# Performance work log

Measured on AMD Instinct MI355X. Metric: run time of the kernel, lower is better.

## Reference

```python
import jax, jax.numpy as jnp
import numpy as np

T, B = 64, 512
X, H, Z, A = 1024, 1024, 256, 64


def setup_inputs() -> dict:
    key = jax.random.key(0)
    ks = jax.random.split(key, 24)
    s = 0.02
    n = lambda k, shape: (jax.random.normal(k, shape, dtype=jnp.float32) * s)
    d = {
        "obs_seq": jax.random.normal(ks[0], (T, B, X), dtype=jnp.float32),
        "act_seq": jax.random.normal(ks[1], (T, B, A), dtype=jnp.float32),
        "eps": jax.random.normal(ks[2], (T, B, Z), dtype=jnp.float32),
        # Transition: aggr Linear(z+a -> h), GRUCell(h, h)
        "aggr_W": n(ks[3], (Z + A, H)), "aggr_b": jnp.zeros((H,), jnp.float32),
        "gru_Wih": n(ks[4], (H, 3 * H)), "gru_Whh": n(ks[5], (H, 3 * H)),
        "gru_bih": jnp.zeros((3 * H,), jnp.float32), "gru_bhh": jnp.zeros((3 * H,), jnp.float32),
        # z_q_dist: NormalPredictor(x+h -> hidden h -> z)
        "q_W1": n(ks[6], (X + H, H)), "q_b1": jnp.zeros((H,), jnp.float32),
        "q_Wm": n(ks[7], (H, Z)), "q_bm": jnp.zeros((Z,), jnp.float32),
        "q_Ws": n(ks[8], (H, Z)), "q_bs": jnp.zeros((Z,), jnp.float32),
        # z_p_dist: NormalPredictor(h -> hidden h -> z)
        "p_W1": n(ks[9], (H, H)), "p_b1": jnp.zeros((H,), jnp.float32),
        "p_Wm": n(ks[10], (H, Z)), "p_bm": jnp.zeros((Z,), jnp.float32),
        "p_Ws": n(ks[11], (H, Z)), "p_bs": jnp.zeros((Z,), jnp.float32),
    }
    return d


def _gru_cell(x, h, Wih, Whh, bih, bhh):
    # torch.nn.GRUCell math
    gi = x @ Wih + bih
    gh = h @ Whh + bhh
    i_r, i_z, i_n = jnp.split(gi, 3, axis=-1)
    h_r, h_z, h_n = jnp.split(gh, 3, axis=-1)
    r = jax.nn.sigmoid(i_r + h_r)
    z = jax.nn.sigmoid(i_z + h_z)
    n = jnp.tanh(i_n + r * h_n)
    return (1.0 - z) * n + z * h


def _normal_predictor(x, W1, b1, Wm, bm, Ws, bs):
    hid = jax.nn.elu(x @ W1 + b1)
    loc = hid @ Wm + bm
    scale = jax.nn.softplus(hid @ Ws + bs)
    return loc, scale


def reference(obs_seq, act_seq, eps, aggr_W, aggr_b, gru_Wih, gru_Whh, gru_bih,
              gru_bhh, q_W1, q_b1, q_Wm, q_bm, q_Ws, q_bs, p_W1, p_b1, p_Wm,
              p_bm, p_Ws, p_bs):
    batch = obs_seq.shape[1]
    h0 = jnp.zeros((batch, gru_Whh.shape[0]), dtype=obs_seq.dtype)

    def step(h, inp):
        obs, act, e = inp
        q_loc, q_scale = _normal_predictor(
            jnp.concatenate([obs, h], axis=-1), q_W1, q_b1, q_Wm, q_bm, q_Ws, q_bs)
        z_q = q_loc + q_scale * e  # rsample
        p_loc, p_scale = _normal_predictor(h, p_W1, p_b1, p_Wm, p_bm, p_Ws, p_bs)
        a = jax.nn.elu(jnp.concatenate([z_q, act], axis=-1) @ aggr_W + aggr_b)
        h_new = _gru_cell(a, h, gru_Wih, gru_Whh, gru_bih, gru_bhh)
        return h_new, (h_new, q_loc, q_scale, p_loc, p_scale, z_q)

    _, (bel, q_loc, q_scale, p_loc, p_scale, z_qs) = jax.lax.scan(
        step, h0, (obs_seq, act_seq, eps))
    beliefs = jnp.concatenate([h0[None], bel], axis=0)  # [T+1, B, H]
    return beliefs, (q_loc, q_scale), (p_loc, p_scale), z_qs
```

## Files before the change

kernel.cpp:

```cpp
#include <hip/hip_runtime.h>
#include <hip/hip_bf16.h>
#include <stdint.h>

#define TT 64
#define BB 512
#define XX 1024
#define HH 1024
#define ZZ 256
#define AA 64

#define NBLK 256
#define NTHR 512
#define ROWS 16
#define RPG 8

typedef __bf16 bf16;
typedef bf16 bf16x8 __attribute__((ext_vector_type(8)));
typedef float f32x4 __attribute__((ext_vector_type(4)));
typedef unsigned int u32x4 __attribute__((ext_vector_type(4)));

#define SZ_BEL ((long)(TT + 1) * BB * HH)
#define SZ_TBZ ((long)TT * BB * ZZ)
#define OFF_QL (SZ_BEL)
#define OFF_QS (OFF_QL + SZ_TBZ)
#define OFF_PL (OFF_QL + 2 * SZ_TBZ)
#define OFF_PS (OFF_QL + 3 * SZ_TBZ)
#define OFF_ZQ (OFF_QL + 4 * SZ_TBZ)

#define GLL16(g, l)                                                         \
  __builtin_amdgcn_global_load_lds(                                         \
      (__attribute__((address_space(1))) void*)(g),                         \
      (__attribute__((address_space(3))) void*)(l), 16, 0, 0)

#define MFMA(a, b, c) __builtin_amdgcn_mfma_f32_16x16x32_bf16(a, b, c, 0, 0, 0)

#define ALOAD_U64(p) __hip_atomic_load((const unsigned long long*)(p), __ATOMIC_RELAXED, __HIP_MEMORY_SCOPE_AGENT)
#define ALOAD_U32(p) __hip_atomic_load((const unsigned*)(p), __ATOMIC_RELAXED, __HIP_MEMORY_SCOPE_AGENT)
#define ASTORE_U16(p, v) __hip_atomic_store((unsigned short*)(p), (v), __ATOMIC_RELAXED, __HIP_MEMORY_SCOPE_AGENT)
#define ASTORE_U64(p, v) __hip_atomic_store((unsigned long long*)(p), (v), __ATOMIC_RELAXED, __HIP_MEMORY_SCOPE_AGENT)
#define ASTORE_U32(p, v) __hip_atomic_store((unsigned*)(p), (v), __ATOMIC_RELAXED, __HIP_MEMORY_SCOPE_AGENT)

__device__ __forceinline__ float eluf(float x) { return x > 0.f ? x : expf(x) - 1.f; }
__device__ __forceinline__ float splusf(float x) { return fmaxf(x, 0.f) + log1pf(expf(-fabsf(x))); }
__device__ __forceinline__ float sigf(float x) { return 1.f / (1.f + expf(-x)); }
__device__ __forceinline__ unsigned short bf2u(bf16 v) { return __builtin_bit_cast(unsigned short, v); }
__device__ __forceinline__ float u2f(unsigned short u) { return (float)__builtin_bit_cast(bf16, u); }
__device__ __forceinline__ bf16x8 ldg8(const bf16* p) { return *(const bf16x8*)p; }

__device__ __forceinline__ void cload16(u32x4& v, const void* p) {
  asm volatile("global_load_dwordx4 %0, %1, off sc0 sc1" : "=v"(v) : "v"(p));
}

__device__ __forceinline__ bf16x8 ldfrag(const char* tile, int row, int w) {
  return *(const bf16x8*)(tile + row * 128 + (w ^ ((row & 7) << 4)));
}

template <int C>
__device__ __forceinline__ void stage_panel16(const bf16* base, char* lds) {
  constexpr int ITER = (2 * C) / NTHR;
  u32x4 v[ITER];
#pragma unroll
  for (int i = 0; i < ITER; ++i) {
    int u = threadIdx.x + i * NTHR;
    int ktile = u >> 7, rem = u & 127;
    int row = rem >> 3, cb = (rem & 7) * 16;
    cload16(v[i], (const char*)base + (long)row * (C * 2) + ktile * 128 + cb);
  }
  asm volatile("s_waitcnt vmcnt(0)" ::: "memory");
  __builtin_amdgcn_sched_barrier(0);
#pragma unroll
  for (int i = 0; i < ITER; ++i) {
    int u = threadIdx.x + i * NTHR;
    int ktile = u >> 7, rem = u & 127;
    int row = rem >> 3, cb = (rem & 7) * 16;
    *(u32x4*)(lds + ktile * 2048 + row * 128 + (cb ^ ((row & 7) << 4))) = v[i];
  }
}

__device__ __forceinline__ void stage_act(const bf16* base, char* lds) {
  if (threadIdx.x < 128) {
    int u = threadIdx.x;
    int row = u >> 3, cb = (u & 7) * 16;
    u32x4 v = *(const u32x4*)((const char*)base + row * 128 + cb);
    *(u32x4*)(lds + row * 128 + (cb ^ ((row & 7) << 4))) = v;
  }
}

__device__ __forceinline__ void gbar(unsigned* arr, unsigned* go, int rank, unsigned gen) {
  __syncthreads();
  if (rank == 0) {
    if (threadIdx.x > 0 && threadIdx.x < RPG) {
      while (ALOAD_U32(&arr[threadIdx.x]) < gen) __builtin_amdgcn_s_sleep(2);
    }
    if (threadIdx.x == 0) ASTORE_U32(go, gen);
  } else if (threadIdx.x == 0) {
    ASTORE_U32(&arr[rank], gen);
    while (ALOAD_U32(go) < gen) __builtin_amdgcn_s_sleep(2);
  }
  __syncthreads();
  asm volatile("" ::: "memory");
}

struct ScanArgs {
  const bf16 *Pq1, *Pqh, *Pag, *Pih, *Phh;
  const bf16 *obs_preT, *act_bf;
  bf16 *h, *hid, *z, *a, *ghT;
  const float *b_q1, *b_ghh, *b_qm, *b_qs, *b_ag, *b_gih;
  const float* eps;
  float* dout;
  unsigned* bar;
};

__global__ __launch_bounds__(NTHR, 2) void scan_k(ScanArgs s) {
  __shared__ __align__(16) char smem[98304];
  const int tid = threadIdx.x;
  const int wid = tid >> 6, lane = tid & 63;
  const int lr = lane & 15, lk = lane >> 4;

  int xcd;
  asm volatile("s_getreg_b32 %0, hwreg(HW_REG_XCC_ID)" : "=s"(xcd));
  xcd &= 7;
  __shared__ int sgr;
  if (tid == 0) sgr = (int)atomicAdd(&s.bar[2048 + xcd * 64], 1u);
  __syncthreads();
  const int rank = xcd;
  const int g = sgr;

  unsigned gen = 0;
  unsigned* arr = s.bar + g * 32;
  unsigned* go = s.bar + 1024 + g * 32;

  bf16* hg = s.h + (long)g * ROWS * HH;
  bf16* hid_g = s.hid + (long)g * ROWS * HH;
  bf16* zg = s.z + (long)g * ROWS * ZZ;
  bf16* ag = s.a + (long)g * ROWS * HH;
  bf16* ghT_g = s.ghT + (long)g * 3072 * ROWS;

  float hreg[4] = {0.f, 0.f, 0.f, 0.f};

  for (int t = 0; t < TT; ++t) {
    {
      stage_panel16<1024>(hg, smem);
      __syncthreads();
      const bool isHid = rank < 2;
      const int fb = (isHid ? rank : rank - 2) * 32 + wid * 4;
      const bf16* P = isHid ? s.Pq1 : s.Phh;
      const bf16* bp[4];
#pragma unroll
      for (int nj = 0; nj < 4; ++nj) bp[nj] = P + ((long)(fb + nj) * 32) * 512 + lane * 8;
      bf16x8 br[2][4];
#pragma unroll
      for (int nj = 0; nj < 4; ++nj) { br[0][nj] = ldg8(bp[nj]); br[1][nj] = ldg8(bp[nj] + 512); }
      f32x4 acc[4] = {};
#pragma unroll
      for (int kk = 0; kk < 32; ++kk) {
        const int sl = kk & 1;
        bf16x8 a = ldfrag(smem + (kk >> 1) * 2048, lr, (kk & 1) * 64 + lk * 16);
#pragma unroll
        for (int nj = 0; nj < 4; ++nj) acc[nj] = MFMA(a, br[sl][nj], acc[nj]);
        if (kk + 2 < 32) {
#pragma unroll
          for (int nj = 0; nj < 4; ++nj) br[sl][nj] = ldg8(bp[nj] + (kk + 2) * 512);
        }
      }
      if (isHid) {
        const int colb = rank * 512 + wid * 64;
#pragma unroll
        for (int nj = 0; nj < 4; ++nj) {
          const int col = colb + nj * 16 + lr;
          const float bq = s.b_q1[col];
          unsigned long long o8 = *(const unsigned long long*)
              &s.obs_preT[((long)t * HH + col) * BB + g * ROWS + lk * 4];
#pragma unroll
          for (int r = 0; r < 4; ++r) {
            float x = acc[nj][r] + bq + u2f((unsigned short)(o8 >> (16 * r)));
            ASTORE_U16(&hid_g[(lk * 4 + r) * HH + col], bf2u((bf16)eluf(x)));
          }
        }
      } else {
        const int colb = (rank - 2) * 512 + wid * 64;
#pragma unroll
        for (int nj = 0; nj < 4; ++nj) {
          const int cg = colb + nj * 16 + lr;
          unsigned long long pk = 0;
#pragma unroll
          for (int r = 0; r < 4; ++r)
            pk |= (unsigned long long)bf2u((bf16)acc[nj][r]) << (16 * r);
          ASTORE_U64(&ghT_g[(long)cg * ROWS + lk * 4], pk);
        }
      }
    }
    gbar(arr, go, rank, ++gen);

    {
      stage_panel16<1024>(hid_g, smem);
      __syncthreads();
      if (wid < 4) {
        const int f = rank * 4 + wid;
        const bf16* bp = s.Pqh + ((long)f * 32) * 512 + lane * 8;
        bf16x8 br[4];
#pragma unroll
        for (int p = 0; p < 4; ++p) br[p] = ldg8(bp + p * 512);
        f32x4 acc = {};
#pragma unroll
        for (int kk = 0; kk < 32; ++kk) {
          bf16x8 a = ldfrag(smem + (kk >> 1) * 2048, lr, (kk & 1) * 64 + lk * 16);
          acc = MFMA(a, br[kk & 3], acc);
          if (kk + 4 < 32) br[kk & 3] = ldg8(bp + (kk + 4) * 512);
        }
        const int j0 = rank * 32 + wid * 8;
        const int jj = j0 + (lr & 7);
        const float bias = (lr < 8) ? s.b_qm[jj] : s.b_qs[jj];
#pragma unroll
        for (int r = 0; r < 4; ++r) {
          const int rl = lk * 4 + r;
          const long grow = (long)g * ROWS + rl;
          const long o = ((long)t * BB + grow) * ZZ + jj;
          float myv = acc[r] + bias;
          float sp = splusf(myv);
          float sc = __shfl(sp, lane + 8, 64);
          if (lr < 8) {
            float zv = myv + sc * s.eps[o];
            s.dout[OFF_QL + o] = myv;
            s.dout[OFF_ZQ + o] = zv;
            ASTORE_U16(&zg[rl * ZZ + jj], bf2u((bf16)zv));
          } else {
            s.dout[OFF_QS + o] = sp;
          }
        }
      }
    }
    gbar(arr, go, rank, ++gen);

    {
      stage_panel16<256>(zg, smem);
      stage_act(s.act_bf + ((long)t * BB + (long)g * ROWS) * AA, smem + 4 * 2048);
      __syncthreads();
      const int f = rank * 8 + wid;
      const bf16* bp = s.Pag + ((long)f * 10) * 512 + lane * 8;
      bf16x8 br[10];
#pragma unroll
      for (int p = 0; p < 10; ++p) br[p] = ldg8(bp + (long)p * 512);
      f32x4 acc = {};
#pragma unroll
      for (int kk = 0; kk < 10; ++kk) {
        bf16x8 a = ldfrag(smem + (kk >> 1) * 2048, lr, (kk & 1) * 64 + lk * 16);
        acc = MFMA(a, br[kk], acc);
      }
      const int col = rank * 128 + wid * 16 + lr;
      const float ba = s.b_ag[col];
#pragma unroll
      for (int r = 0; r < 4; ++r)
        ASTORE_U16(&ag[(lk * 4 + r) * HH + col], bf2u((bf16)eluf(acc[r] + ba)));
    }
    gbar(arr, go, rank, ++gen);

    {
      const int j = rank * 128 + wid * 16 + lr;
      unsigned long long ghp0 = ALOAD_U64(&ghT_g[(long)(0 * HH + j) * ROWS + lk * 4]);
      unsigned long long ghp1 = ALOAD_U64(&ghT_g[(long)(1 * HH + j) * ROWS + lk * 4]);
      unsigned long long ghp2 = ALOAD_U64(&ghT_g[(long)(2 * HH + j) * ROWS + lk * 4]);
      stage_panel16<1024>(ag, smem);
      __syncthreads();
      const int fb = rank * 8 + wid;
      const bf16* bp0 = s.Pih + ((long)(0 * 64 + fb) * 32) * 512 + lane * 8;
      const bf16* bp1 = s.Pih + ((long)(1 * 64 + fb) * 32) * 512 + lane * 8;
      const bf16* bp2 = s.Pih + ((long)(2 * 64 + fb) * 32) * 512 + lane * 8;
      bf16x8 b0[2], b1[2], b2[2];
      b0[0] = ldg8(bp0); b0[1] = ldg8(bp0 + 512);
      b1[0] = ldg8(bp1); b1[1] = ldg8(bp1 + 512);
      b2[0] = ldg8(bp2); b2[1] = ldg8(bp2 + 512);
      f32x4 gi0 = {}, gi1 = {}, gi2 = {};
#pragma unroll
      for (int kk = 0; kk < 32; ++kk) {
        const int sl = kk & 1;
        bf16x8 a = ldfrag(smem + (kk >> 1) * 2048, lr, (kk & 1) * 64 + lk * 16);
        gi0 = MFMA(a, b0[sl], gi0);
        gi1 = MFMA(a, b1[sl], gi1);
        gi2 = MFMA(a, b2[sl], gi2);
        if (kk + 2 < 32) {
          b0[sl] = ldg8(bp0 + (kk + 2) * 512);
          b1[sl] = ldg8(bp1 + (kk + 2) * 512);
          b2[sl] = ldg8(bp2 + (kk + 2) * 512);
        }
      }
      const float bi0 = s.b_gih[j], bi1 = s.b_gih[HH + j], bi2 = s.b_gih[2 * HH + j];
      const float bh0 = s.b_ghh[j], bh1 = s.b_ghh[HH + j], bh2 = s.b_ghh[2 * HH + j];
#pragma unroll
      for (int r = 0; r < 4; ++r) {
        const int rl = lk * 4 + r;
        float rr = sigf(gi0[r] + bi0 + u2f((unsigned short)(ghp0 >> (16 * r))) + bh0);
        float zz = sigf(gi1[r] + bi1 + u2f((unsigned short)(ghp1 >> (16 * r))) + bh1);
        float nn = tanhf(gi2[r] + bi2 + rr * (u2f((unsigned short)(ghp2 >> (16 * r))) + bh2));
        float hnew = (1.f - zz) * nn + zz * hreg[r];
        hreg[r] = hnew;
        ASTORE_U16(&hg[rl * HH + j], bf2u((bf16)hnew));
        s.dout[(long)(t + 1) * BB * HH + ((long)g * ROWS + rl) * HH + j] = hnew;
      }
    }
    gbar(arr, go, rank, ++gen);
  }
}

__global__ void pack16(const float* __restrict__ W, bf16* __restrict__ dst,
                       int ld, int row0, int kts, int kmax, long total) {
  long idx = (long)blockIdx.x * 256 + threadIdx.x;
  if (idx >= total) return;
  int l = (int)(idx & 63);
  long fk = idx >> 6;
  int kt = (int)(fk % kts);
  int f = (int)(fk / kts);
  int col = f * 16 + (l & 15);
  int k = kt * 32 + (l >> 4) * 8;
  bf16x8 v;
#pragma unroll
  for (int e = 0; e < 8; ++e) {
    int kk = k + e;
    v[e] = (bf16)((kk < kmax) ? W[(long)(row0 + kk) * ld + col] : 0.f);
  }
  *(bf16x8*)&dst[idx * 8] = v;
}

__global__ void pack_qh(const float* __restrict__ Wm, const float* __restrict__ Ws,
                        bf16* __restrict__ dst) {
  long idx = (long)blockIdx.x * 256 + threadIdx.x;
  int l = (int)(idx & 63);
  long fk = idx >> 6;
  int f = (int)(fk >> 5);
  int k = (int)((fk & 31) * 32) + (l >> 4) * 8;
  const float* W = ((l & 15) < 8) ? Wm : Ws;
  int col = f * 8 + (l & 7);
  bf16x8 v;
#pragma unroll
  for (int e = 0; e < 8; ++e) v[e] = (bf16)W[(long)(k + e) * 256 + col];
  *(bf16x8*)&dst[idx * 8] = v;
}


struct GArgs {
  const bf16* A; const float* Af;
  long lda;
  const bf16* Bt;
  int M, N, K;
  const float *b_p1, *b_pm, *b_ps;
  bf16* out_bf;
  float* dout;
};

template <int BM, int BN, int EPI, bool AF32>
__global__ __launch_bounds__(256) void gemm_k(GArgs g) {
  constexpr int BK = 32;
  constexpr int WTM = BM / 2, WTN = BN / 2;
  constexpr int MR = WTM / 16, NR = WTN / 16;
  constexpr int CA = BM * 4 / 256, CB = BN * 4 / 256;
  __shared__ bf16 sA[BM * BK];
  __shared__ bf16 sB[BN * BK];
  const int nbm = g.M / BM;
  const int bm = blockIdx.x % nbm, bn = blockIdx.x / nbm;
  const int m0 = bm * BM, n0 = bn * BN;
  const int tid = threadIdx.x;
  const int wid = tid >> 6, lane = tid & 63;
  const int wm = wid & 1, wn = wid >> 1;
  const int lr = lane & 15, lk = lane >> 4;

  f32x4 acc[MR][NR] = {};

  for (int k0 = 0; k0 < g.K; k0 += BK) {
    __syncthreads();
    if constexpr (AF32) {
#pragma unroll
      for (int i = 0; i < CA; i++) {
        int c = tid + i * 256, row = c >> 2, kc = c & 3;
        const float* sp = g.Af + (long)(m0 + row) * g.lda + k0 + kc * 8;
        float4 v0 = *(const float4*)sp;
        float4 v1 = *(const float4*)(sp + 4);
        bf16x8 p;
        p[0] = (bf16)v0.x; p[1] = (bf16)v0.y; p[2] = (bf16)v0.z; p[3] = (bf16)v0.w;
        p[4] = (bf16)v1.x; p[5] = (bf16)v1.y; p[6] = (bf16)v1.z; p[7] = (bf16)v1.w;
        *(bf16x8*)&sA[c * 8] = p;
      }
    } else {
#pragma unroll
      for (int i = 0; i < CA; i++) {
        int c = tid + i * 256, row = c >> 2, kc = c & 3;
        GLL16(g.A + (long)(m0 + row) * g.lda + k0 + kc * 8, &sA[c * 8]);
      }
    }
#pragma unroll
    for (int i = 0; i < CB; i++) {
      int c = tid + i * 256, row = c >> 2, kc = c & 3;
      GLL16(g.Bt + (long)(n0 + row) * g.K + k0 + kc * 8, &sB[c * 8]);
    }
    __syncthreads();
    bf16x8 af[MR];
#pragma unroll
    for (int mi = 0; mi < MR; mi++)
      af[mi] = *(const bf16x8*)&sA[(wm * WTM + mi * 16 + lr) * BK + lk * 8];
#pragma unroll
    for (int nj = 0; nj < NR; nj++) {
      bf16x8 bfr = *(const bf16x8*)&sB[(wn * WTN + nj * 16 + lr) * BK + lk * 8];
#pragma unroll
      for (int mi = 0; mi < MR; mi++)
        acc[mi][nj] = MFMA(af[mi], bfr, acc[mi][nj]);
    }
  }

#pragma unroll
  for (int mi = 0; mi < MR; mi++)
#pragma unroll
    for (int nj = 0; nj < NR; nj++)
#pragma unroll
      for (int r = 0; r < 4; r++) {
        const int row = m0 + wm * WTM + mi * 16 + lk * 4 + r;
        const int col = n0 + wn * WTN + nj * 16 + lr;
        float v = acc[mi][nj][r];
        if constexpr (EPI == 7) {
          g.out_bf[((long)(row >> 9) * HH + col) * BB + (row & 511)] = (bf16)v;
        } else if constexpr (EPI == 5) {
          g.out_bf[(long)row * g.N + col] = (bf16)eluf(v + g.b_p1[col]);
        } else {
          int region = col >> 8, j = col & 255;
          float x = v + (region ? g.b_ps[j] : g.b_pm[j]);
          if (region) x = splusf(x);
          g.dout[(region ? OFF_PS : OFF_PL) + (long)row * ZZ + j] = x;
        }
      }
}

__global__ void transpose_cvt(const float* __restrict__ src, bf16* __restrict__ dst,
                              int K, int N, int ld, int k_off) {
  __shared__ float tile[32][33];
  const int nb = blockIdx.x * 32, kb = blockIdx.y * 32;
  const int tx = threadIdx.x, ty = threadIdx.y;
#pragma unroll
  for (int j = 0; j < 32; j += 8)
    tile[ty + j][tx] = src[(long)(kb + ty + j + k_off) * ld + nb + tx];
  __syncthreads();
#pragma unroll
  for (int j = 0; j < 32; j += 8)
    dst[(long)(nb + ty + j) * K + kb + tx] = (bf16)tile[tx][ty + j];
}

__global__ void cvt_bf16(const float* __restrict__ src, bf16* __restrict__ dst, long n) {
  long i = ((long)blockIdx.x * blockDim.x + threadIdx.x) * 4;
  if (i < n) {
    float4 v = *(const float4*)(src + i);
    dst[i] = (bf16)v.x; dst[i + 1] = (bf16)v.y;
    dst[i + 2] = (bf16)v.z; dst[i + 3] = (bf16)v.w;
  }
}

__global__ void init_k(bf16* hbf, float* dout) {
  int i = blockIdx.x * 256 + threadIdx.x;
  hbf[i] = (bf16)0.f;
  dout[i] = 0.f;
}

extern "C" void kernel_launch(void* const* d_in, const int* in_sizes, int n_in,
                              void* d_out, int out_size, void* d_ws, size_t ws_size,
                              hipStream_t stream) {
  const float* obs  = (const float*)d_in[0];
  const float* act  = (const float*)d_in[1];
  const float* eps  = (const float*)d_in[2];
  const float* aggrW = (const float*)d_in[3];
  const float* aggrB = (const float*)d_in[4];
  const float* gWih = (const float*)d_in[5];
  const float* gWhh = (const float*)d_in[6];
  const float* gbih = (const float*)d_in[7];
  const float* gbhh = (const float*)d_in[8];
  const float* qW1  = (const float*)d_in[9];
  const float* qb1  = (const float*)d_in[10];
  const float* qWm  = (const float*)d_in[11];
  const float* qbm  = (const float*)d_in[12];
  const float* qWs  = (const float*)d_in[13];
  const float* qbs  = (const float*)d_in[14];
  const float* pW1  = (const float*)d_in[15];
  const float* pb1  = (const float*)d_in[16];
  const float* pWm  = (const float*)d_in[17];
  const float* pbm  = (const float*)d_in[18];
  const float* pWs  = (const float*)d_in[19];
  const float* pbs  = (const float*)d_in[20];
  float* dout = (float*)d_out;

  char* w = (char*)d_ws;
  size_t off = 0;
  auto alloc = [&](size_t bytes) -> char* {
    char* r = w + off;
    off = (off + bytes + 255) & ~(size_t)255;
    return r;
  };
  bf16* Pq1 = (bf16*)alloc((size_t)64 * 32 * 512 * 2);
  bf16* Pqh = (bf16*)alloc((size_t)32 * 32 * 512 * 2);
  bf16* Pag = (bf16*)alloc((size_t)64 * 10 * 512 * 2);
  bf16* Pih = (bf16*)alloc((size_t)192 * 32 * 512 * 2);
  bf16* Phh = (bf16*)alloc((size_t)192 * 32 * 512 * 2);
  bf16* WT_qobs = (bf16*)alloc((size_t)XX * HH * 2);
  bf16* WT_p1  = (bf16*)alloc((size_t)HH * HH * 2);
  bf16* WT_ph  = (bf16*)alloc((size_t)512 * HH * 2);
  bf16* obs_preT = (bf16*)alloc((size_t)TT * HH * BB * 2);
  bf16* p_hid  = obs_preT;
  bf16* act_bf = (bf16*)alloc((size_t)TT * BB * AA * 2);
  bf16* h_bf   = (bf16*)alloc((size_t)BB * HH * 2);
  bf16* hid_q  = (bf16*)alloc((size_t)BB * HH * 2);
  bf16* z_bf   = (bf16*)alloc((size_t)BB * ZZ * 2);
  bf16* a_buf  = (bf16*)alloc((size_t)BB * HH * 2);
  bf16* ghT    = (bf16*)alloc((size_t)BB * 3 * HH * 2);
  unsigned* bar = (unsigned*)alloc(16384);
  (void)ws_size; (void)in_sizes; (void)n_in; (void)out_size;

  hipMemsetAsync(bar, 0, 16384, stream);

  pack16<<<512, 256, 0, stream>>>(qW1, Pq1, 1024, 1024, 32, 1024, 64L * 32 * 64);
  pack16<<<1536, 256, 0, stream>>>(gWhh, Phh, 3072, 0, 32, 1024, 192L * 32 * 64);
  pack16<<<1536, 256, 0, stream>>>(gWih, Pih, 3072, 0, 32, 1024, 192L * 32 * 64);
  pack16<<<160, 256, 0, stream>>>(aggrW, Pag, 1024, 0, 10, 320, 64L * 10 * 64);
  pack_qh<<<256, 256, 0, stream>>>(qWm, qWs, Pqh);

  dim3 tb(32, 8);
  transpose_cvt<<<dim3(32, 32), tb, 0, stream>>>(qW1, WT_qobs, 1024, 1024, 1024, 0);
  transpose_cvt<<<dim3(32, 32), tb, 0, stream>>>(pW1, WT_p1, 1024, 1024, 1024, 0);
  transpose_cvt<<<dim3(8, 32), tb, 0, stream>>>(pWm, WT_ph, 1024, 256, 256, 0);
  transpose_cvt<<<dim3(8, 32), tb, 0, stream>>>(pWs, WT_ph + 256 * 1024, 1024, 256, 256, 0);
  cvt_bf16<<<TT * BB * AA / 4 / 256, 256, 0, stream>>>(act, act_bf, (long)TT * BB * AA);
  init_k<<<BB * HH / 256, 256, 0, stream>>>(h_bf, dout);

  {
    GArgs a{};
    a.Af = obs; a.lda = XX; a.Bt = WT_qobs;
    a.M = TT * BB; a.N = HH; a.K = XX; a.out_bf = obs_preT;
    gemm_k<128, 128, 7, true><<<(TT * BB / 128) * (HH / 128), 256, 0, stream>>>(a);
  }

  {
    ScanArgs s{};
    s.Pq1 = Pq1; s.Pqh = Pqh; s.Pag = Pag; s.Pih = Pih; s.Phh = Phh;
    s.obs_preT = obs_preT; s.act_bf = act_bf;
    s.h = h_bf; s.hid = hid_q; s.z = z_bf; s.a = a_buf; s.ghT = ghT;
    s.b_q1 = qb1; s.b_ghh = gbhh; s.b_qm = qbm; s.b_qs = qbs;
    s.b_ag = aggrB; s.b_gih = gbih;
    s.eps = eps; s.dout = dout; s.bar = bar;
    scan_k<<<NBLK, NTHR, 0, stream>>>(s);
  }

  {
    GArgs a{};
    a.Af = dout; a.lda = HH; a.Bt = WT_p1;
    a.M = TT * BB; a.N = HH; a.K = HH; a.out_bf = p_hid; a.b_p1 = pb1;
    gemm_k<128, 128, 5, true><<<(TT * BB / 128) * (HH / 128), 256, 0, stream>>>(a);
  }
  {
    GArgs a{};
    a.A = p_hid; a.lda = HH; a.Bt = WT_ph;
    a.M = TT * BB; a.N = 512; a.K = HH;
    a.b_pm = pbm; a.b_ps = pbs; a.dout = dout;
    gemm_k<128, 128, 6, false><<<(TT * BB / 128) * (512 / 128), 256, 0, stream>>>(a);
  }
}
```

Measured before the change: 8.152 ms.

## Stage per-step operands contiguously into LDS with coalesced bypass loads

Replaces the scattered per-thread global reads of h/hid/a panels, obs preactivations, eps and GRU hidden-gate values with contiguous 64-byte-per-thread loads into LDS staging buffers, read back from LDS in the epilogues. The obs-projection GEMM epilogue now writes a group-blocked layout ([group][t][col][16 rows]) so each group's step slice is contiguous. This is meant to cut uncoalesced, latency-bound global traffic inside the serial scan steps. The trade-off is that fewer threads issue the staging loads and extra LDS space and barriers are needed, with padded LDS strides to avoid bank conflicts.

```diff
diff --git a/kernel.cpp b/kernel.cpp
--- a/kernel.cpp
+++ b/kernel.cpp
@@ -34,7 +34,6 @@
 
 #define MFMA(a, b, c) __builtin_amdgcn_mfma_f32_16x16x32_bf16(a, b, c, 0, 0, 0)
 
-#define ALOAD_U64(p) __hip_atomic_load((const unsigned long long*)(p), __ATOMIC_RELAXED, __HIP_MEMORY_SCOPE_AGENT)
 #define ALOAD_U32(p) __hip_atomic_load((const unsigned*)(p), __ATOMIC_RELAXED, __HIP_MEMORY_SCOPE_AGENT)
 #define ASTORE_U16(p, v) __hip_atomic_store((unsigned short*)(p), (v), __ATOMIC_RELAXED, __HIP_MEMORY_SCOPE_AGENT)
 #define ASTORE_U64(p, v) __hip_atomic_store((unsigned long long*)(p), (v), __ATOMIC_RELAXED, __HIP_MEMORY_SCOPE_AGENT)
@@ -56,33 +55,38 @@
 }
 
 template <int C>
-__device__ __forceinline__ void stage_panel16(const bf16* base, char* lds) {
-  constexpr int ITER = (2 * C) / NTHR;
-  u32x4 v[ITER];
-#pragma unroll
-  for (int i = 0; i < ITER; ++i) {
-    int u = threadIdx.x + i * NTHR;
-    int ktile = u >> 7, rem = u & 127;
-    int row = rem >> 3, cb = (rem & 7) * 16;
-    cload16(v[i], (const char*)base + (long)row * (C * 2) + ktile * 128 + cb);
-  }
-  asm volatile("s_waitcnt vmcnt(0)" ::: "memory");
-  __builtin_amdgcn_sched_barrier(0);
-#pragma unroll
-  for (int i = 0; i < ITER; ++i) {
-    int u = threadIdx.x + i * NTHR;
-    int ktile = u >> 7, rem = u & 127;
-    int row = rem >> 3, cb = (rem & 7) * 16;
-    *(u32x4*)(lds + ktile * 2048 + row * 128 + (cb ^ ((row & 7) << 4))) = v[i];
+__device__ __forceinline__ void stage_bypass(const bf16* base, char* lds) {
+  constexpr int THR = (2 * C) / 4;
+  if (threadIdx.x < THR) {
+    u32x4 v[4];
+#pragma unroll
+    for (int i = 0; i < 4; ++i)
+      cload16(v[i], (const char*)base + (threadIdx.x * 4 + i) * 16);
+    asm volatile("s_waitcnt vmcnt(0)" ::: "memory");
+    __builtin_amdgcn_sched_barrier(0);
+#pragma unroll
+    for (int i = 0; i < 4; ++i) {
+      int gb = (threadIdx.x * 4 + i) * 16;
+      int row = (C == 1024) ? (gb >> 11) : (gb >> 9);
+      int colb = gb & (2 * C - 1);
+      int ktile = colb >> 7, cb = colb & 127;
+      *(u32x4*)(lds + ktile * 2048 + row * 128 + (cb ^ ((row & 7) << 4))) = v[i];
+    }
   }
 }
 
 __device__ __forceinline__ void stage_act(const bf16* base, char* lds) {
-  if (threadIdx.x < 128) {
-    int u = threadIdx.x;
-    int row = u >> 3, cb = (u & 7) * 16;
-    u32x4 v = *(const u32x4*)((const char*)base + row * 128 + cb);
-    *(u32x4*)(lds + row * 128 + (cb ^ ((row & 7) << 4))) = v;
+  if (threadIdx.x < 32) {
+    u32x4 v[4];
+#pragma unroll
+    for (int i = 0; i < 4; ++i)
+      v[i] = *(const u32x4*)((const char*)base + (threadIdx.x * 4 + i) * 16);
+#pragma unroll
+    for (int i = 0; i < 4; ++i) {
+      int u = threadIdx.x * 4 + i;
+      int row = u >> 3, cb = (u & 7) * 16;
+      *(u32x4*)(lds + row * 128 + (cb ^ ((row & 7) << 4))) = v[i];
+    }
   }
 }
 
@@ -103,7 +107,7 @@
 
 struct ScanArgs {
   const bf16 *Pq1, *Pqh, *Pag, *Pih, *Phh;
-  const bf16 *obs_preT, *act_bf;
+  const bf16 *obs_pre, *act_bf;
   bf16 *h, *hid, *z, *a, *ghT;
   const float *b_q1, *b_ghh, *b_qm, *b_qs, *b_ag, *b_gih;
   const float* eps;
@@ -113,6 +117,7 @@
 
 __global__ __launch_bounds__(NTHR, 2) void scan_k(ScanArgs s) {
   __shared__ __align__(16) char smem[98304];
+  char* aux = smem + 32768;
   const int tid = threadIdx.x;
   const int wid = tid >> 6, lane = tid & 63;
   const int lr = lane & 15, lk = lane >> 4;
@@ -140,9 +145,21 @@
 
   for (int t = 0; t < TT; ++t) {
     {
-      stage_panel16<1024>(hg, smem);
+      const bool isHid = rank < 2;
+      stage_bypass<1024>(hg, smem);
+      if (isHid && tid < 256) {
+        const char* gb = (const char*)(s.obs_pre +
+            (((long)g * TT + t) * HH + rank * 512) * 16);
+        u32x4 v[4];
+#pragma unroll
+        for (int i = 0; i < 4; ++i) v[i] = *(const u32x4*)(gb + (tid * 4 + i) * 16);
+#pragma unroll
+        for (int i = 0; i < 4; ++i) {
+          int u = tid * 4 + i;
+          *(u32x4*)(aux + (u >> 1) * 40 + (u & 1) * 16) = v[i];
+        }
+      }
       __syncthreads();
-      const bool isHid = rank < 2;
       const int fb = (isHid ? rank : rank - 2) * 32 + wid * 4;
       const bf16* P = isHid ? s.Pq1 : s.Phh;
       const bf16* bp[4];
@@ -170,7 +187,7 @@
           const int col = colb + nj * 16 + lr;
           const float bq = s.b_q1[col];
           unsigned long long o8 = *(const unsigned long long*)
-              &s.obs_preT[((long)t * HH + col) * BB + g * ROWS + lk * 4];
+              (aux + (wid * 64 + nj * 16 + lr) * 40 + lk * 8);
 #pragma unroll
           for (int r = 0; r < 4; ++r) {
             float x = acc[nj][r] + bq + u2f((unsigned short)(o8 >> (16 * r)));
@@ -193,7 +210,15 @@
     gbar(arr, go, rank, ++gen);
 
     {
-      stage_panel16<1024>(hid_g, smem);
+      stage_bypass<1024>(hid_g, smem);
+      if (tid < 256) {
+        const char* gb = (const char*)(s.eps + ((long)t * BB + (long)g * ROWS) * ZZ);
+        u32x4 v[4];
+#pragma unroll
+        for (int i = 0; i < 4; ++i) v[i] = *(const u32x4*)(gb + (tid * 4 + i) * 16);
+#pragma unroll
+        for (int i = 0; i < 4; ++i) *(u32x4*)(aux + (tid * 4 + i) * 16) = v[i];
+      }
       __syncthreads();
       if (wid < 4) {
         const int f = rank * 4 + wid;
@@ -220,7 +245,8 @@
           float sp = splusf(myv);
           float sc = __shfl(sp, lane + 8, 64);
           if (lr < 8) {
-            float zv = myv + sc * s.eps[o];
+            float ev = *(const float*)(aux + ((long)rl * ZZ + jj) * 4);
+            float zv = myv + sc * ev;
             s.dout[OFF_QL + o] = myv;
             s.dout[OFF_ZQ + o] = zv;
             ASTORE_U16(&zg[rl * ZZ + jj], bf2u((bf16)zv));
@@ -233,7 +259,7 @@
     gbar(arr, go, rank, ++gen);
 
     {
-      stage_panel16<256>(zg, smem);
+      stage_bypass<256>(zg, smem);
       stage_act(s.act_bf + ((long)t * BB + (long)g * ROWS) * AA, smem + 4 * 2048);
       __syncthreads();
       const int f = rank * 8 + wid;
@@ -256,11 +282,22 @@
     gbar(arr, go, rank, ++gen);
 
     {
-      const int j = rank * 128 + wid * 16 + lr;
-      unsigned long long ghp0 = ALOAD_U64(&ghT_g[(long)(0 * HH + j) * ROWS + lk * 4]);
-      unsigned long long ghp1 = ALOAD_U64(&ghT_g[(long)(1 * HH + j) * ROWS + lk * 4]);
-      unsigned long long ghp2 = ALOAD_U64(&ghT_g[(long)(2 * HH + j) * ROWS + lk * 4]);
-      stage_panel16<1024>(ag, smem);
+      stage_bypass<1024>(ag, smem);
+      if (tid < 192) {
+        u32x4 v[4];
+        const int gate = (tid * 4) >> 8;
+        const int uin = (tid * 4) & 255;
+        const char* gb = (const char*)(ghT_g + ((long)gate * 1024 + rank * 128) * 16);
+#pragma unroll
+        for (int i = 0; i < 4; ++i) cload16(v[i], gb + (uin + i) * 16);
+        asm volatile("s_waitcnt vmcnt(0)" ::: "memory");
+        __builtin_amdgcn_sched_barrier(0);
+#pragma unroll
+        for (int i = 0; i < 4; ++i) {
+          int u = uin + i;
+          *(u32x4*)(aux + gate * 5120 + (u >> 1) * 40 + (u & 1) * 16) = v[i];
+        }
+      }
       __syncthreads();
       const int fb = rank * 8 + wid;
       const bf16* bp0 = s.Pih + ((long)(0 * 64 + fb) * 32) * 512 + lane * 8;
@@ -284,6 +321,11 @@
           b2[sl] = ldg8(bp2 + (kk + 2) * 512);
         }
       }
+      const int j = rank * 128 + wid * 16 + lr;
+      const int jrel = wid * 16 + lr;
+      unsigned long long ghp0 = *(const unsigned long long*)(aux + 0 * 5120 + jrel * 40 + lk * 8);
+      unsigned long long ghp1 = *(const unsigned long long*)(aux + 1 * 5120 + jrel * 40 + lk * 8);
+      unsigned long long ghp2 = *(const unsigned long long*)(aux + 2 * 5120 + jrel * 40 + lk * 8);
       const float bi0 = s.b_gih[j], bi1 = s.b_gih[HH + j], bi2 = s.b_gih[2 * HH + j];
       const float bh0 = s.b_ghh[j], bh1 = s.b_ghh[HH + j], bh2 = s.b_ghh[2 * HH + j];
 #pragma unroll
@@ -415,7 +457,8 @@
         const int col = n0 + wn * WTN + nj * 16 + lr;
         float v = acc[mi][nj][r];
         if constexpr (EPI == 7) {
-          g.out_bf[((long)(row >> 9) * HH + col) * BB + (row & 511)] = (bf16)v;
+          const int brow = row & 511, tt = row >> 9;
+          g.out_bf[((((long)(brow >> 4) * TT + tt) * HH + col) << 4) + (brow & 15)] = (bf16)v;
         } else if constexpr (EPI == 5) {
           g.out_bf[(long)row * g.N + col] = (bf16)eluf(v + g.b_p1[col]);
         } else {
@@ -497,8 +540,8 @@
   bf16* WT_qobs = (bf16*)alloc((size_t)XX * HH * 2);
   bf16* WT_p1  = (bf16*)alloc((size_t)HH * HH * 2);
   bf16* WT_ph  = (bf16*)alloc((size_t)512 * HH * 2);
-  bf16* obs_preT = (bf16*)alloc((size_t)TT * HH * BB * 2);
-  bf16* p_hid  = obs_preT;
+  bf16* obs_pre = (bf16*)alloc((size_t)TT * HH * BB * 2);
+  bf16* p_hid  = obs_pre;
   bf16* act_bf = (bf16*)alloc((size_t)TT * BB * AA * 2);
   bf16* h_bf   = (bf16*)alloc((size_t)BB * HH * 2);
   bf16* hid_q  = (bf16*)alloc((size_t)BB * HH * 2);
@@ -527,14 +570,14 @@
   {
     GArgs a{};
     a.Af = obs; a.lda = XX; a.Bt = WT_qobs;
-    a.M = TT * BB; a.N = HH; a.K = XX; a.out_bf = obs_preT;
+    a.M = TT * BB; a.N = HH; a.K = XX; a.out_bf = obs_pre;
     gemm_k<128, 128, 7, true><<<(TT * BB / 128) * (HH / 128), 256, 0, stream>>>(a);
   }
 
   {
     ScanArgs s{};
     s.Pq1 = Pq1; s.Pqh = Pqh; s.Pag = Pag; s.Pih = Pih; s.Phh = Phh;
-    s.obs_preT = obs_preT; s.act_bf = act_bf;
+    s.obs_pre = obs_pre; s.act_bf = act_bf;
     s.h = h_bf; s.hid = hid_q; s.z = z_bf; s.a = a_buf; s.ghT = ghT;
     s.b_q1 = qb1; s.b_ghh = gbhh; s.b_qm = qbm; s.b_qs = qbs;
     s.b_ag = aggrB; s.b_gih = gbih;
```

Result: no change. 8.247 ms (+1.2%).
